# Performance work log

Hardware: AMD Instinct MI355X
Metric: run time of the kernel (lower is better)

Reference implementation:

```python
import jax, jax.numpy as jnp
import numpy as np

D = 512; H = 8; DH = D // H; DFF = 4 * D; INNER = 2 * D; K = 31
B = 8; S = 1024
EPS = 1e-5


def layer_norm(x, g, b):
    m = jnp.mean(x, axis=-1, keepdims=True)
    v = jnp.mean(jnp.square(x - m), axis=-1, keepdims=True)
    return (x - m) * jax.lax.rsqrt(v + EPS) * g + b


def setup_inputs() -> dict:
    key = jax.random.key(0)
    ks = iter(jax.random.split(key, 32))
    w = lambda *s: jax.random.normal(next(ks), s, dtype=jnp.float32) * 0.02
    d = {
        "x": jax.random.normal(next(ks), (B, S, D), dtype=jnp.float32),
        # FF module 1
        "ln1_g": jnp.ones((D,)), "ln1_b": jnp.zeros((D,)),
        "ff1_w1": w(DFF, D), "ff1_b1": jnp.zeros((DFF,)),
        "ff1_w2": w(D, DFF), "ff1_b2": jnp.zeros((D,)),
        # attention
        "lna_g": jnp.ones((D,)), "lna_b": jnp.zeros((D,)),
        "qkv_w": w(3 * D, D), "qkv_b": jnp.zeros((3 * D,)),
        "out_w": w(D, D), "out_b": jnp.zeros((D,)),
        # conv module
        "lnc_g": jnp.ones((D,)), "lnc_b": jnp.zeros((D,)),
        "pw1_w": w(INNER, D), "pw1_b": jnp.zeros((INNER,)),
        "dw_w": w(D, 1, K), "dw_b": jnp.zeros((D,)),
        "bn_g": jnp.ones((D,)), "bn_b": jnp.zeros((D,)),
        "bn_mean": jnp.zeros((D,)), "bn_var": jnp.ones((D,)),
        "pw2_w": w(D, D), "pw2_b": jnp.zeros((D,)),
        # FF module 2
        "ln2_g": jnp.ones((D,)), "ln2_b": jnp.zeros((D,)),
        "ff2_w1": w(DFF, D), "ff2_b1": jnp.zeros((DFF,)),
        "ff2_w2": w(D, DFF), "ff2_b2": jnp.zeros((D,)),
        # final layer norm
        "lnf_g": jnp.ones((D,)), "lnf_b": jnp.zeros((D,)),
    }
    return d


def _ff(x, g, b, w1, b1, w2, b2):
    h = layer_norm(x, g, b)
    h = jax.nn.silu(h @ w1.T + b1)
    h = h @ w2.T + b2
    return h + x  # FeedForwardModule adds its own residual


def _attn(x, g, b, qkv_w, qkv_b, out_w, out_b):
    h = layer_norm(x, g, b)
    qkv = (h @ qkv_w.T + qkv_b).reshape(B, S, 3, H, DH)
    q, k, v = qkv[:, :, 0], qkv[:, :, 1], qkv[:, :, 2]  # [B,S,H,DH]
    scores = jnp.einsum('bqhd,bkhd->bhqk', q, k) / np.sqrt(DH).astype(np.float32)
    probs = jax.nn.softmax(scores, axis=-1)
    ctx = jnp.einsum('bhqk,bkhd->bqhd', probs, v).reshape(B, S, D)
    return ctx @ out_w.T + out_b


def _conv(x, g, b, pw1_w, pw1_b, dw_w, dw_b, bn_g, bn_b, bn_mean, bn_var, pw2_w, pw2_b):
    h = layer_norm(x, g, b)
    y = h @ pw1_w.T + pw1_b                      # [B,S,2D] pointwise conv1
    a, gate = jnp.split(y, 2, axis=-1)           # GLU along channel dim
    y = a * jax.nn.sigmoid(gate)                 # [B,S,D]
    y = y.transpose(0, 2, 1)                     # [B,D,S]
    y = jax.lax.conv_general_dilated(
        y, dw_w, window_strides=(1,), padding=((K // 2, K // 2),),
        dimension_numbers=('NCH', 'OIH', 'NCH'), feature_group_count=D)
    y = y + dw_b[None, :, None]
    y = (y - bn_mean[None, :, None]) * jax.lax.rsqrt(bn_var + EPS)[None, :, None]
    y = y * bn_g[None, :, None] + bn_b[None, :, None]
    y = jax.nn.silu(y)
    y = y.transpose(0, 2, 1)                     # [B,S,D]
    y = y @ pw2_w.T + pw2_b
    return y + x  # ConvModule adds its own residual


def reference(x, ln1_g, ln1_b, ff1_w1, ff1_b1, ff1_w2, ff1_b2,
              lna_g, lna_b, qkv_w, qkv_b, out_w, out_b,
              lnc_g, lnc_b, pw1_w, pw1_b, dw_w, dw_b,
              bn_g, bn_b, bn_mean, bn_var, pw2_w, pw2_b,
              ln2_g, ln2_b, ff2_w1, ff2_b1, ff2_w2, ff2_b2,
              lnf_g, lnf_b):
    x = x + 0.5 * _ff(x, ln1_g, ln1_b, ff1_w1, ff1_b1, ff1_w2, ff1_b2)
    x = x + _attn(x, lna_g, lna_b, qkv_w, qkv_b, out_w, out_b)
    x = x + _conv(x, lnc_g, lnc_b, pw1_w, pw1_b, dw_w, dw_b,
                  bn_g, bn_b, bn_mean, bn_var, pw2_w, pw2_b)
    x = x + 0.5 * _ff(x, ln2_g, ln2_b, ff2_w1, ff2_b1, ff2_w2, ff2_b2)
    return layer_norm(x, lnf_g, lnf_b)
```

## Files before the change

### kernel.cpp

```cpp
#include <hip/hip_runtime.h>
#include <hip/hip_bf16.h>

typedef __attribute__((ext_vector_type(8))) short bf16x8;
typedef __attribute__((ext_vector_type(4))) float f32x4;

#define NTOK 8192
#define SEQ  1024
#define NH   8

__device__ __forceinline__ float bfs2f(short s) {
  union { unsigned u; float f; } x; x.u = ((unsigned)(unsigned short)s) << 16; return x.f;
}
__device__ __forceinline__ short f2bfs(float f) {
  __hip_bfloat16 h = __float2bfloat16(f);
  return *reinterpret_cast<short*>(&h);
}
__device__ __forceinline__ float bfp2f(const __hip_bfloat16* p) {
  return bfs2f(*reinterpret_cast<const short*>(p));
}

__device__ __forceinline__ void gld16(const void* g, void* l) {
  __builtin_amdgcn_global_load_lds(
      (__attribute__((address_space(1))) void*)const_cast<void*>(g),
      (__attribute__((address_space(3))) void*)l, 16, 0, 0);
}

__global__ __launch_bounds__(256) void cvt_x_kernel(const float* __restrict__ xin,
                                                    float* __restrict__ xs) {
  const size_t i = ((size_t)blockIdx.x * 256 + threadIdx.x) * 8;
  *reinterpret_cast<f32x4*>(xs + i)     = *reinterpret_cast<const f32x4*>(xin + i);
  *reinterpret_cast<f32x4*>(xs + i + 4) = *reinterpret_cast<const f32x4*>(xin + i + 4);
}

struct WSeg { const float* src; unsigned dst_off; unsigned nvec; };
struct WPack { WSeg s[8]; };

__global__ __launch_bounds__(256) void cast_wall_kernel(WPack p,
                                                        __hip_bfloat16* __restrict__ dst) {
  unsigned v = blockIdx.x * 256 + threadIdx.x;
#pragma unroll
  for (int t = 0; t < 8; ++t) {
    if (v < p.s[t].nvec) {
      const float* s = p.s[t].src + (size_t)v * 8;
      f32x4 a = *reinterpret_cast<const f32x4*>(s);
      f32x4 b = *reinterpret_cast<const f32x4*>(s + 4);
      bf16x8 o;
#pragma unroll
      for (int j = 0; j < 4; ++j) { o[j] = f2bfs(a[j]); o[4 + j] = f2bfs(b[j]); }
      *reinterpret_cast<bf16x8*>(reinterpret_cast<short*>(dst) +
                                 (size_t)(p.s[t].dst_off + v) * 8) = o;
      return;
    }
    v -= p.s[t].nvec;
  }
}

__global__ __launch_bounds__(256) void cast_dww_kernel(const float* __restrict__ src,
                                                       __hip_bfloat16* __restrict__ dst) {
  for (int k = 0; k < 31; ++k)
    for (int c = threadIdx.x; c < 512; c += 256)
      dst[k * 512 + c] = __float2bfloat16(src[c * 31 + k]);
}

struct PtrPack { const void* p[23]; };

__global__ __launch_bounds__(256) void cast_small_kernel(PtrPack pk,
                                                         __hip_bfloat16* __restrict__ dst) {
  constexpr int sizes[23] = {512, 512, 2048, 512, 512, 512, 1536, 512, 512, 512, 1024, 512,
                             512, 512, 512, 512, 512, 512, 512, 2048, 512, 512, 512};
  int off = 0;
  for (int t = 0; t < 23; ++t) {
    const int n = sizes[t];
    for (int i = threadIdx.x; i < n; i += 256)
      dst[off + i] = __float2bfloat16(((const float*)pk.p[t])[i]);
    off += n;
  }
}

__global__ void ws_bad_kernel(float* __restrict__ out) {
  if (threadIdx.x == 0) out[0] = 5000.f;
}

__global__ __launch_bounds__(256) void ln_kernel(const float* __restrict__ in,
                                                 const __hip_bfloat16* __restrict__ g,
                                                 const __hip_bfloat16* __restrict__ b,
                                                 __hip_bfloat16* __restrict__ out) {
  const int wv = threadIdx.x >> 6, ln = threadIdx.x & 63;
  const int row = blockIdx.x * 4 + wv;
  const float* p = in + (size_t)row * 512 + ln * 8;
  float v[8];
  {
    const f32x4* p4 = reinterpret_cast<const f32x4*>(p);
    f32x4 a = p4[0], c = p4[1];
#pragma unroll
    for (int j = 0; j < 4; ++j) { v[j] = a[j]; v[4 + j] = c[j]; }
  }
  float s = 0.f;
#pragma unroll
  for (int j = 0; j < 8; ++j) s += v[j];
  for (int m = 1; m < 64; m <<= 1) s += __shfl_xor(s, m);
  const float mean = s * (1.f / 512.f);
  float q = 0.f;
#pragma unroll
  for (int j = 0; j < 8; ++j) { float d = v[j] - mean; q += d * d; }
  for (int m = 1; m < 64; m <<= 1) q += __shfl_xor(q, m);
  const float rstd = rsqrtf(q * (1.f / 512.f) + 1e-5f);
  bf16x8 gg = *reinterpret_cast<const bf16x8*>(g + ln * 8);
  bf16x8 bb = *reinterpret_cast<const bf16x8*>(b + ln * 8);
  bf16x8 ov;
#pragma unroll
  for (int j = 0; j < 8; ++j)
    ov[j] = f2bfs((v[j] - mean) * rstd * bfs2f(gg[j]) + bfs2f(bb[j]));
  *reinterpret_cast<bf16x8*>(out + (size_t)row * 512 + ln * 8) = ov;
}

__global__ __launch_bounds__(256) void lnf_kernel(const float* __restrict__ in,
                                                  const __hip_bfloat16* __restrict__ g,
                                                  const __hip_bfloat16* __restrict__ b,
                                                  float* __restrict__ out) {
  const int wv = threadIdx.x >> 6, ln = threadIdx.x & 63;
  const int row = blockIdx.x * 4 + wv;
  const float* p = in + (size_t)row * 512 + ln * 8;
  float v[8];
  {
    const f32x4* p4 = reinterpret_cast<const f32x4*>(p);
    f32x4 a = p4[0], c = p4[1];
#pragma unroll
    for (int j = 0; j < 4; ++j) { v[j] = a[j]; v[4 + j] = c[j]; }
  }
  float s = 0.f;
#pragma unroll
  for (int j = 0; j < 8; ++j) s += v[j];
  for (int m = 1; m < 64; m <<= 1) s += __shfl_xor(s, m);
  const float mean = s * (1.f / 512.f);
  float q = 0.f;
#pragma unroll
  for (int j = 0; j < 8; ++j) { float d = v[j] - mean; q += d * d; }
  for (int m = 1; m < 64; m <<= 1) q += __shfl_xor(q, m);
  const float rstd = rsqrtf(q * (1.f / 512.f) + 1e-5f);
  bf16x8 gg = *reinterpret_cast<const bf16x8*>(g + ln * 8);
  bf16x8 bb = *reinterpret_cast<const bf16x8*>(b + ln * 8);
  f32x4 o0, o1;
#pragma unroll
  for (int j = 0; j < 4; ++j) {
    o0[j] = (v[j] - mean) * rstd * bfs2f(gg[j]) + bfs2f(bb[j]);
    o1[j] = (v[4 + j] - mean) * rstd * bfs2f(gg[4 + j]) + bfs2f(bb[4 + j]);
  }
  float* op = out + (size_t)row * 512 + ln * 8;
  *reinterpret_cast<f32x4*>(op) = o0;
  *reinterpret_cast<f32x4*>(op + 4) = o1;
}

template <int EPI>
__global__ __launch_bounds__(256, 2) void gemm_bt(const __hip_bfloat16* __restrict__ A,
                                                  const __hip_bfloat16* __restrict__ W,
                                                  const __hip_bfloat16* __restrict__ bias,
                                                  __hip_bfloat16* __restrict__ outb,
                                                  float* __restrict__ resid,
                                                  int K, int M, float alpha, float beta) {
  __shared__ __align__(16) __hip_bfloat16 As[128 * 64];
  __shared__ __align__(16) __hip_bfloat16 Bs[128 * 64];
  const int tid = threadIdx.x;
  const int wv = tid >> 6, ln = tid & 63;
  const int hi = ln >> 4, lo = ln & 15;
  const int n0 = blockIdx.x * 128;
  const int m0 = blockIdx.y * 128;
  const int wr = wv >> 1, wc = wv & 1;
  const int srow = ln >> 3;
  const int scol = (ln & 7) * 8;

  f32x4 acc[4][4] = {};

  for (int k0 = 0; k0 < K; k0 += 64) {
    __syncthreads();
#pragma unroll
    for (int i = 0; i < 4; ++i) {
      const int grp = i * 4 + wv;
      const int row = grp * 8 + srow;
      gld16(A + (size_t)(n0 + row) * K + k0 + scol, As + grp * 512);
      gld16(W + (size_t)(m0 + row) * K + k0 + scol, Bs + grp * 512);
    }
    __syncthreads();
#pragma unroll
    for (int kk = 0; kk < 64; kk += 32) {
      bf16x8 af[4], bfr[4];
#pragma unroll
      for (int r = 0; r < 4; ++r)
        af[r] = *reinterpret_cast<const bf16x8*>(As + (wr * 64 + r * 16 + lo) * 64 + kk + hi * 8);
#pragma unroll
      for (int c = 0; c < 4; ++c)
        bfr[c] = *reinterpret_cast<const bf16x8*>(Bs + (wc * 64 + c * 16 + lo) * 64 + kk + hi * 8);
#pragma unroll
      for (int r = 0; r < 4; ++r)
#pragma unroll
        for (int c = 0; c < 4; ++c)
          acc[r][c] = __builtin_amdgcn_mfma_f32_16x16x32_bf16(af[r], bfr[c], acc[r][c], 0, 0, 0);
    }
  }

#pragma unroll
  for (int r = 0; r < 4; ++r) {
#pragma unroll
    for (int c = 0; c < 4; ++c) {
      const int m = m0 + wc * 64 + c * 16 + lo;
      const float bv = bfp2f(bias + m);
#pragma unroll
      for (int j = 0; j < 4; ++j) {
        const int n = n0 + wr * 64 + r * 16 + hi * 4 + j;
        float v = acc[r][c][j] + bv;
        if constexpr (EPI == 1) v = v / (1.f + __expf(-v));
        if constexpr (EPI <= 1) {
          outb[(size_t)n * M + m] = __float2bfloat16(v);
        } else {
          const size_t idx = (size_t)n * 512 + m;
          resid[idx] = alpha * resid[idx] + beta * v;
        }
      }
    }
  }
}

__global__ __launch_bounds__(256, 4) void gemm64_resid(const __hip_bfloat16* __restrict__ A,
                                                       const __hip_bfloat16* __restrict__ W,
                                                       const __hip_bfloat16* __restrict__ bias,
                                                       float* __restrict__ resid,
                                                       int K, float alpha, float beta) {
  __shared__ __align__(16) __hip_bfloat16 As[64 * 64];
  __shared__ __align__(16) __hip_bfloat16 Bs[128 * 64];
  const int tid = threadIdx.x;
  const int wv = tid >> 6, ln = tid & 63;
  const int hi = ln >> 4, lo = ln & 15;
  const int n0 = blockIdx.x * 64;
  const int m0 = blockIdx.y * 128;
  const int wr = wv >> 1, wc = wv & 1;
  const int srow = ln >> 3;
  const int scol = (ln & 7) * 8;

  f32x4 acc[2][4] = {};

  for (int k0 = 0; k0 < K; k0 += 64) {
    __syncthreads();
#pragma unroll
    for (int i = 0; i < 2; ++i) {
      const int grp = i * 4 + wv;
      gld16(A + (size_t)(n0 + grp * 8 + srow) * K + k0 + scol, As + grp * 512);
    }
#pragma unroll
    for (int i = 0; i < 4; ++i) {
      const int grp = i * 4 + wv;
      gld16(W + (size_t)(m0 + grp * 8 + srow) * K + k0 + scol, Bs + grp * 512);
    }
    __syncthreads();
#pragma unroll
    for (int kk = 0; kk < 64; kk += 32) {
      bf16x8 af[2], bfr[4];
#pragma unroll
      for (int r = 0; r < 2; ++r)
        af[r] = *reinterpret_cast<const bf16x8*>(As + (wr * 32 + r * 16 + lo) * 64 + kk + hi * 8);
#pragma unroll
      for (int c = 0; c < 4; ++c)
        bfr[c] = *reinterpret_cast<const bf16x8*>(Bs + (wc * 64 + c * 16 + lo) * 64 + kk + hi * 8);
#pragma unroll
      for (int r = 0; r < 2; ++r)
#pragma unroll
        for (int c = 0; c < 4; ++c)
          acc[r][c] = __builtin_amdgcn_mfma_f32_16x16x32_bf16(af[r], bfr[c], acc[r][c], 0, 0, 0);
    }
  }

#pragma unroll
  for (int r = 0; r < 2; ++r) {
#pragma unroll
    for (int c = 0; c < 4; ++c) {
      const int m = m0 + wc * 64 + c * 16 + lo;
      const float bv = bfp2f(bias + m);
#pragma unroll
      for (int j = 0; j < 4; ++j) {
        const int n = n0 + wr * 32 + r * 16 + hi * 4 + j;
        const size_t idx = (size_t)n * 512 + m;
        resid[idx] = alpha * resid[idx] + beta * (acc[r][c][j] + bv);
      }
    }
  }
}

__global__ __launch_bounds__(256, 1) void naive_attn_kernel(
    const __hip_bfloat16* __restrict__ qkv, __hip_bfloat16* __restrict__ ctx) {
  const int idx = blockIdx.x * 256 + threadIdx.x;
  const int b = idx >> 13;
  const int h = (idx >> 10) & 7;
  const int q = idx & 1023;
  const __hip_bfloat16* qp = qkv + (size_t)(b * SEQ + q) * 1536 + h * 64;
  float qreg[64];
#pragma unroll
  for (int j8 = 0; j8 < 8; ++j8) {
    bf16x8 v = *reinterpret_cast<const bf16x8*>(qp + j8 * 8);
#pragma unroll
    for (int jj = 0; jj < 8; ++jj) qreg[j8 * 8 + jj] = bfs2f(v[jj]);
  }
  float m = -1e30f, l = 0.f;
  float acc[64];
#pragma unroll
  for (int d = 0; d < 64; ++d) acc[d] = 0.f;
  for (int k = 0; k < SEQ; ++k) {
    const __hip_bfloat16* kp = qkv + (size_t)(b * SEQ + k) * 1536 + 512 + h * 64;
    float dot = 0.f;
#pragma unroll
    for (int j8 = 0; j8 < 8; ++j8) {
      bf16x8 v = *reinterpret_cast<const bf16x8*>(kp + j8 * 8);
#pragma unroll
      for (int jj = 0; jj < 8; ++jj) dot += qreg[j8 * 8 + jj] * bfs2f(v[jj]);
    }
    const float s = dot * 0.125f;
    const float nm = fmaxf(m, s);
    const float resc = __expf(m - nm);
    const float p = __expf(s - nm);
    l = l * resc + p;
    const __hip_bfloat16* vp = qkv + (size_t)(b * SEQ + k) * 1536 + 1024 + h * 64;
#pragma unroll
    for (int j8 = 0; j8 < 8; ++j8) {
      bf16x8 v = *reinterpret_cast<const bf16x8*>(vp + j8 * 8);
#pragma unroll
      for (int jj = 0; jj < 8; ++jj)
        acc[j8 * 8 + jj] = acc[j8 * 8 + jj] * resc + p * bfs2f(v[jj]);
    }
    m = nm;
  }
  __hip_bfloat16* op = ctx + (size_t)(b * SEQ + q) * 512 + h * 64;
  const float rl = 1.f / l;
#pragma unroll
  for (int j8 = 0; j8 < 8; ++j8) {
    bf16x8 o;
#pragma unroll
    for (int jj = 0; jj < 8; ++jj) o[jj] = f2bfs(acc[j8 * 8 + jj] * rl);
    *reinterpret_cast<bf16x8*>(op + j8 * 8) = o;
  }
}

__global__ __launch_bounds__(256) void vtrans_kernel(const __hip_bfloat16* __restrict__ qkv,
                                                     __hip_bfloat16* __restrict__ vT) {
  __shared__ __hip_bfloat16 tile[64][65];
  const int bh = blockIdx.x;
  const int s0 = blockIdx.y * 64;
  const int b = bh >> 3, h = bh & 7;
  const int c = threadIdx.x & 63;
  const int r4 = threadIdx.x >> 6;
#pragma unroll
  for (int i = 0; i < 16; ++i) {
    const int s = r4 * 16 + i;
    tile[s][c] = qkv[(size_t)(b * 1024 + s0 + s) * 1536 + 1024 + h * 64 + c];
  }
  __syncthreads();
#pragma unroll
  for (int i = 0; i < 16; ++i) {
    const int d = r4 * 16 + i;
    vT[((size_t)bh * 64 + d) * 1024 + s0 + c] = tile[c][d];
  }
}

__global__ __launch_bounds__(256, 4) void attn_kernel(const __hip_bfloat16* __restrict__ qkv,
                                                      const __hip_bfloat16* __restrict__ vT,
                                                      __hip_bfloat16* __restrict__ ctx) {
  __shared__ __align__(16) short Ks[2][64 * 64];
  __shared__ __align__(16) short Vs[2][64 * 64];
  __shared__ __align__(16) short P[4][16][64];
  const int tid = threadIdx.x;
  const int wv = tid >> 6, ln = tid & 63;
  const int hi = ln >> 4, lo = ln & 15;
  const int lo7 = lo & 7;
  const int blk = ((blockIdx.x & 7) << 7) | (blockIdx.x >> 3);
  const int qt = blk & 15, h = (blk >> 4) & 7, b = blk >> 7;
  const int q0 = qt * 64 + wv * 16;
  const float scale = 0.125f;

  const int srow8 = ln >> 3;
  const int gsrc = (ln & 7) ^ srow8;

  const __hip_bfloat16* qp = qkv + (size_t)(b * SEQ + q0 + lo) * 1536 + h * 64 + hi * 8;
  bf16x8 aq0 = *reinterpret_cast<const bf16x8*>(qp);
  bf16x8 aq1 = *reinterpret_cast<const bf16x8*>(qp + 32);

  const __hip_bfloat16* kbase = qkv + 512 + h * 64 + (size_t)b * SEQ * 1536;
  const __hip_bfloat16* vbase = vT + (size_t)(b * NH + h) * 64 * 1024;

  f32x4 oacc[4] = {};
  float mrow[4] = {-1e30f, -1e30f, -1e30f, -1e30f};
  float lrow[4] = {0.f, 0.f, 0.f, 0.f};

#pragma unroll
  for (int c = 0; c < 2; ++c) {
    const int r = c * 32 + wv * 8 + srow8;
    gld16(kbase + (size_t)r * 1536 + gsrc * 8, &Ks[0][(c * 32 + wv * 8) * 64]);
    gld16(vbase + (size_t)r * 1024 + gsrc * 8, &Vs[0][(c * 32 + wv * 8) * 64]);
  }
  __syncthreads();

  int cb = 0;
  for (int kt = 0; kt < 16; ++kt) {
    if (kt < 15) {
      const int kb2 = (kt + 1) * 64;
#pragma unroll
      for (int c = 0; c < 2; ++c) {
        const int r = c * 32 + wv * 8 + srow8;
        gld16(kbase + (size_t)(kb2 + r) * 1536 + gsrc * 8,
              &Ks[cb ^ 1][(c * 32 + wv * 8) * 64]);
        gld16(vbase + (size_t)r * 1024 + kb2 + gsrc * 8,
              &Vs[cb ^ 1][(c * 32 + wv * 8) * 64]);
      }
    }

    f32x4 sc[4] = {};
#pragma unroll
    for (int nt = 0; nt < 4; ++nt) {
      const short* kr = &Ks[cb][(nt * 16 + lo) * 64];
      bf16x8 bk0 = *reinterpret_cast<const bf16x8*>(kr + ((hi ^ lo7) << 3));
      bf16x8 bk1 = *reinterpret_cast<const bf16x8*>(kr + (((hi + 4) ^ lo7) << 3));
      sc[nt] = __builtin_amdgcn_mfma_f32_16x16x32_bf16(aq0, bk0, sc[nt], 0, 0, 0);
      sc[nt] = __builtin_amdgcn_mfma_f32_16x16x32_bf16(aq1, bk1, sc[nt], 0, 0, 0);
    }

#pragma unroll
    for (int j = 0; j < 4; ++j) {
      float v = fmaxf(fmaxf(sc[0][j], sc[1][j]), fmaxf(sc[2][j], sc[3][j])) * scale;
      v = fmaxf(v, __shfl_xor(v, 1));
      v = fmaxf(v, __shfl_xor(v, 2));
      v = fmaxf(v, __shfl_xor(v, 4));
      v = fmaxf(v, __shfl_xor(v, 8));
      const float nm = fmaxf(mrow[j], v);
      const float resc = __expf(mrow[j] - nm);
      mrow[j] = nm;
      const int prow = hi * 4 + j;
      const int pswz = (prow & 7) << 3;
      float rs = 0.f;
#pragma unroll
      for (int nt = 0; nt < 4; ++nt) {
        const float p = __expf(sc[nt][j] * scale - nm);
        P[wv][prow][(nt * 16 + lo) ^ pswz] = f2bfs(p);
        rs += p;
      }
      rs += __shfl_xor(rs, 1);
      rs += __shfl_xor(rs, 2);
      rs += __shfl_xor(rs, 4);
      rs += __shfl_xor(rs, 8);
      lrow[j] = lrow[j] * resc + rs;
#pragma unroll
      for (int dt = 0; dt < 4; ++dt) oacc[dt][j] *= resc;
    }
    __syncthreads();

    const short* pr = &P[wv][lo][0];
    bf16x8 ap0 = *reinterpret_cast<const bf16x8*>(pr + ((hi ^ lo7) << 3));
    bf16x8 ap1 = *reinterpret_cast<const bf16x8*>(pr + (((hi + 4) ^ lo7) << 3));
#pragma unroll
    for (int dt = 0; dt < 4; ++dt) {
      const short* vr = &Vs[cb][(dt * 16 + lo) * 64];
      bf16x8 bv0 = *reinterpret_cast<const bf16x8*>(vr + ((hi ^ lo7) << 3));
      bf16x8 bv1 = *reinterpret_cast<const bf16x8*>(vr + (((hi + 4) ^ lo7) << 3));
      oacc[dt] = __builtin_amdgcn_mfma_f32_16x16x32_bf16(ap0, bv0, oacc[dt], 0, 0, 0);
      oacc[dt] = __builtin_amdgcn_mfma_f32_16x16x32_bf16(ap1, bv1, oacc[dt], 0, 0, 0);
    }
    __syncthreads();
    cb ^= 1;
  }
#pragma unroll
  for (int dt = 0; dt < 4; ++dt)
#pragma unroll
    for (int j = 0; j < 4; ++j) {
      const int n = b * SEQ + q0 + hi * 4 + j;
      const int d = h * 64 + dt * 16 + lo;
      ctx[(size_t)n * 512 + d] = __float2bfloat16(oacc[dt][j] / lrow[j]);
    }
}

__global__ __launch_bounds__(256) void glu8_kernel(const __hip_bfloat16* __restrict__ y,
                                                   __hip_bfloat16* __restrict__ o) {
  const int i = blockIdx.x * 256 + threadIdx.x;
  const int c8 = i & 63;
  const int n = i >> 6;
  const short* yp = reinterpret_cast<const short*>(y) + (size_t)n * 1024 + c8 * 8;
  bf16x8 a = *reinterpret_cast<const bf16x8*>(yp);
  bf16x8 g = *reinterpret_cast<const bf16x8*>(yp + 512);
  bf16x8 ov;
#pragma unroll
  for (int j = 0; j < 8; ++j) {
    const float av = bfs2f(a[j]);
    const float gv = bfs2f(g[j]);
    ov[j] = f2bfs(av / (1.f + __expf(-gv)));
  }
  *reinterpret_cast<bf16x8*>(reinterpret_cast<short*>(o) + (size_t)n * 512 + c8 * 8) = ov;
}

__global__ __launch_bounds__(256) void dwconv8_kernel(const __hip_bfloat16* __restrict__ cin,
                                                      const __hip_bfloat16* __restrict__ wkT,
                                                      const __hip_bfloat16* __restrict__ cb,
                                                      const __hip_bfloat16* __restrict__ bng,
                                                      const __hip_bfloat16* __restrict__ bnb,
                                                      const __hip_bfloat16* __restrict__ bnm,
                                                      const __hip_bfloat16* __restrict__ bnv,
                                                      __hip_bfloat16* __restrict__ outp) {
  const int i = blockIdx.x * 256 + threadIdx.x;
  const int c8 = i & 63;
  const int n = i >> 6;
  const int t = n & 1023;
  const int base = n - t;
  const int co = c8 * 8;

  float acc[8];
  {
    bf16x8 bv = *reinterpret_cast<const bf16x8*>(cb + co);
#pragma unroll
    for (int j = 0; j < 8; ++j) acc[j] = bfs2f(bv[j]);
  }
  const int k0 = (t >= 15) ? 0 : (15 - t);
  const int k1 = (t <= SEQ - 16) ? 31 : (SEQ - 1 - t + 16);
  const short* cin_s = reinterpret_cast<const short*>(cin);
  const short* wk_s = reinterpret_cast<const short*>(wkT);
  for (int k = k0; k < k1; ++k) {
    const int ts = t + k - 15;
    bf16x8 xv = *reinterpret_cast<const bf16x8*>(cin_s + (((size_t)(base + ts)) << 9) + co);
    bf16x8 wv = *reinterpret_cast<const bf16x8*>(wk_s + k * 512 + co);
#pragma unroll
    for (int j = 0; j < 8; ++j) acc[j] += bfs2f(xv[j]) * bfs2f(wv[j]);
  }
  bf16x8 g = *reinterpret_cast<const bf16x8*>(bng + co);
  bf16x8 bb = *reinterpret_cast<const bf16x8*>(bnb + co);
  bf16x8 bm = *reinterpret_cast<const bf16x8*>(bnm + co);
  bf16x8 bvv = *reinterpret_cast<const bf16x8*>(bnv + co);
  bf16x8 ov;
#pragma unroll
  for (int j = 0; j < 8; ++j) {
    const float scl = bfs2f(g[j]) * rsqrtf(bfs2f(bvv[j]) + 1e-5f);
    float v = (acc[j] - bfs2f(bm[j])) * scl + bfs2f(bb[j]);
    v = v / (1.f + __expf(-v));
    ov[j] = f2bfs(v);
  }
  *reinterpret_cast<bf16x8*>(reinterpret_cast<short*>(outp) + ((size_t)n << 9) + co) = ov;
}

extern "C" void kernel_launch(void* const* d_in, const int* in_sizes, int n_in,
                              void* d_out, int out_size, void* d_ws, size_t ws_size,
                              hipStream_t stream) {
  float* out = (float*)d_out;
  if (ws_size < ((size_t)80 << 20)) {
    ws_bad_kernel<<<1, 64, 0, stream>>>(out);
    return;
  }

  char* ws = (char*)d_ws;
  float*          xs = (float*)ws;
  __hip_bfloat16* t0 = (__hip_bfloat16*)(ws + ((size_t)16 << 20));
  __hip_bfloat16* t1 = (__hip_bfloat16*)(ws + ((size_t)24 << 20));
  __hip_bfloat16* t2 = (__hip_bfloat16*)(ws + ((size_t)56 << 20));
  __hip_bfloat16* wc = (__hip_bfloat16*)(ws + ((size_t)64 << 20));
  __hip_bfloat16* vT = t1 + (size_t)NTOK * 1536;

  __hip_bfloat16* wc_ff1_w1 = wc + 0;
  __hip_bfloat16* wc_ff1_w2 = wc + 1048576;
  __hip_bfloat16* wc_qkv_w  = wc + 2097152;
  __hip_bfloat16* wc_out_w  = wc + 2883584;
  __hip_bfloat16* wc_pw1_w  = wc + 3145728;
  __hip_bfloat16* wc_pw2_w  = wc + 3670016;
  __hip_bfloat16* wc_ff2_w1 = wc + 3932160;
  __hip_bfloat16* wc_ff2_w2 = wc + 4980736;
  __hip_bfloat16* wc_dwT    = wc + 6029312;
  __hip_bfloat16* sm        = wc + 6045184;
  __hip_bfloat16* c_ln1_g = sm + 0,     *c_ln1_b = sm + 512,   *c_ff1_b1 = sm + 1024;
  __hip_bfloat16* c_ff1_b2 = sm + 3072, *c_lna_g = sm + 3584,  *c_lna_b = sm + 4096;
  __hip_bfloat16* c_qkv_b = sm + 4608,  *c_out_b = sm + 6144,  *c_lnc_g = sm + 6656;
  __hip_bfloat16* c_lnc_b = sm + 7168,  *c_pw1_b = sm + 7680,  *c_dw_b = sm + 8704;
  __hip_bfloat16* c_bn_g = sm + 9216,   *c_bn_b = sm + 9728,   *c_bn_m = sm + 10240;
  __hip_bfloat16* c_bn_v = sm + 10752,  *c_pw2_b = sm + 11264, *c_ln2_g = sm + 11776;
  __hip_bfloat16* c_ln2_b = sm + 12288, *c_ff2_b1 = sm + 12800, *c_ff2_b2 = sm + 14848;
  __hip_bfloat16* c_lnf_g = sm + 15360, *c_lnf_b = sm + 15872;

  cvt_x_kernel<<<2048, 256, 0, stream>>>((const float*)d_in[0], xs);
  {
    WPack wp;
    wp.s[0] = {(const float*)d_in[3],  0,      131072};
    wp.s[1] = {(const float*)d_in[5],  131072, 131072};
    wp.s[2] = {(const float*)d_in[9],  262144, 98304};
    wp.s[3] = {(const float*)d_in[11], 360448, 32768};
    wp.s[4] = {(const float*)d_in[15], 393216, 65536};
    wp.s[5] = {(const float*)d_in[23], 458752, 32768};
    wp.s[6] = {(const float*)d_in[27], 491520, 131072};
    wp.s[7] = {(const float*)d_in[29], 622592, 131072};
    cast_wall_kernel<<<2944, 256, 0, stream>>>(wp, wc);
  }
  cast_dww_kernel<<<1, 256, 0, stream>>>((const float*)d_in[17], wc_dwT);
  PtrPack pk;
  const int small_idx[23] = {1, 2, 4, 6, 7, 8, 10, 12, 13, 14, 16, 18,
                             19, 20, 21, 22, 24, 25, 26, 28, 30, 31, 32};
  for (int t = 0; t < 23; ++t) pk.p[t] = d_in[small_idx[t]];
  cast_small_kernel<<<1, 256, 0, stream>>>(pk, sm);

  ln_kernel<<<2048, 256, 0, stream>>>(xs, c_ln1_g, c_ln1_b, t0);
  gemm_bt<1><<<dim3(64, 16), 256, 0, stream>>>(t0, wc_ff1_w1, c_ff1_b1, t1, nullptr, 512, 2048, 0.f, 0.f);
  gemm64_resid<<<dim3(128, 4), 256, 0, stream>>>(t1, wc_ff1_w2, c_ff1_b2, xs, 2048, 1.5f, 0.5f);

  ln_kernel<<<2048, 256, 0, stream>>>(xs, c_lna_g, c_lna_b, t0);
  gemm_bt<0><<<dim3(64, 12), 256, 0, stream>>>(t0, wc_qkv_w, c_qkv_b, t1, nullptr, 512, 1536, 0.f, 0.f);
  vtrans_kernel<<<dim3(64, 16), 256, 0, stream>>>(t1, vT);
  attn_kernel<<<1024, 256, 0, stream>>>(t1, vT, t2);
  gemm64_resid<<<dim3(128, 4), 256, 0, stream>>>(t2, wc_out_w, c_out_b, xs, 512, 1.0f, 1.0f);

  ln_kernel<<<2048, 256, 0, stream>>>(xs, c_lnc_g, c_lnc_b, t0);
  gemm_bt<0><<<dim3(64, 8), 256, 0, stream>>>(t0, wc_pw1_w, c_pw1_b, t1, nullptr, 512, 1024, 0.f, 0.f);
  glu8_kernel<<<2048, 256, 0, stream>>>(t1, t2);
  dwconv8_kernel<<<2048, 256, 0, stream>>>(t2, wc_dwT, c_dw_b, c_bn_g, c_bn_b, c_bn_m, c_bn_v, t0);
  gemm64_resid<<<dim3(128, 4), 256, 0, stream>>>(t0, wc_pw2_w, c_pw2_b, xs, 512, 2.0f, 1.0f);

  ln_kernel<<<2048, 256, 0, stream>>>(xs, c_ln2_g, c_ln2_b, t0);
  gemm_bt<1><<<dim3(64, 16), 256, 0, stream>>>(t0, wc_ff2_w1, c_ff2_b1, t1, nullptr, 512, 2048, 0.f, 0.f);
  gemm64_resid<<<dim3(128, 4), 256, 0, stream>>>(t1, wc_ff2_w2, c_ff2_b2, xs, 2048, 1.5f, 0.5f);

  lnf_kernel<<<2048, 256, 0, stream>>>(xs, c_lnf_g, c_lnf_b, out);
}
```

Measured before the change: 358.0 us.

## Drop input copy, remap GEMM workgroups per XCD, prescale Q, relax attention barrier

Removes the kernel that copied x into the residual workspace. The first LayerNorm and the first residual GEMM now read the input directly, using a new source pointer so the residual can be read from one buffer and written to another. Both GEMM kernels remap workgroup IDs so that consecutive tiles land on the same XCD, aiming for better L2 reuse of A and W tiles. In attention, Q is prescaled by 1/8 in bf16 at load, which drops per-score multiplies but adds a rounding step. A __syncthreads before reading P is replaced by a compiler-only barrier, relying on each wave reading only its own P slice.

```diff
diff --git a/kernel.cpp b/kernel.cpp
--- a/kernel.cpp
+++ b/kernel.cpp
@@ -23,13 +23,6 @@
   __builtin_amdgcn_global_load_lds(
       (__attribute__((address_space(1))) void*)const_cast<void*>(g),
       (__attribute__((address_space(3))) void*)l, 16, 0, 0);
-}
-
-__global__ __launch_bounds__(256) void cvt_x_kernel(const float* __restrict__ xin,
-                                                    float* __restrict__ xs) {
-  const size_t i = ((size_t)blockIdx.x * 256 + threadIdx.x) * 8;
-  *reinterpret_cast<f32x4*>(xs + i)     = *reinterpret_cast<const f32x4*>(xin + i);
-  *reinterpret_cast<f32x4*>(xs + i + 4) = *reinterpret_cast<const f32x4*>(xin + i + 4);
 }
 
 struct WSeg { const float* src; unsigned dst_off; unsigned nvec; };
@@ -163,8 +156,12 @@
   const int tid = threadIdx.x;
   const int wv = tid >> 6, ln = tid & 63;
   const int hi = ln >> 4, lo = ln & 15;
-  const int n0 = blockIdx.x * 128;
-  const int m0 = blockIdx.y * 128;
+  const int gx = gridDim.x;
+  const int nwg = gx * gridDim.y;
+  const int t = blockIdx.y * gx + blockIdx.x;
+  const int w = (t & 7) * (nwg >> 3) + (t >> 3);
+  const int n0 = (w & (gx - 1)) * 128;
+  const int m0 = (w / gx) * 128;
   const int wr = wv >> 1, wc = wv & 1;
   const int srow = ln >> 3;
   const int scol = (ln & 7) * 8;
@@ -223,6 +220,7 @@
 __global__ __launch_bounds__(256, 4) void gemm64_resid(const __hip_bfloat16* __restrict__ A,
                                                        const __hip_bfloat16* __restrict__ W,
                                                        const __hip_bfloat16* __restrict__ bias,
+                                                       const float* __restrict__ rsrc,
                                                        float* __restrict__ resid,
                                                        int K, float alpha, float beta) {
   __shared__ __align__(16) __hip_bfloat16 As[64 * 64];
@@ -230,8 +228,12 @@
   const int tid = threadIdx.x;
   const int wv = tid >> 6, ln = tid & 63;
   const int hi = ln >> 4, lo = ln & 15;
-  const int n0 = blockIdx.x * 64;
-  const int m0 = blockIdx.y * 128;
+  const int gx = gridDim.x;
+  const int nwg = gx * gridDim.y;
+  const int t = blockIdx.y * gx + blockIdx.x;
+  const int w = (t & 7) * (nwg >> 3) + (t >> 3);
+  const int n0 = (w & (gx - 1)) * 64;
+  const int m0 = (w / gx) * 128;
   const int wr = wv >> 1, wc = wv & 1;
   const int srow = ln >> 3;
   const int scol = (ln & 7) * 8;
@@ -278,7 +280,7 @@
       for (int j = 0; j < 4; ++j) {
         const int n = n0 + wr * 32 + r * 16 + hi * 4 + j;
         const size_t idx = (size_t)n * 512 + m;
-        resid[idx] = alpha * resid[idx] + beta * (acc[r][c][j] + bv);
+        resid[idx] = alpha * rsrc[idx] + beta * (acc[r][c][j] + bv);
       }
     }
   }
@@ -371,14 +373,21 @@
   const int blk = ((blockIdx.x & 7) << 7) | (blockIdx.x >> 3);
   const int qt = blk & 15, h = (blk >> 4) & 7, b = blk >> 7;
   const int q0 = qt * 64 + wv * 16;
-  const float scale = 0.125f;
 
   const int srow8 = ln >> 3;
   const int gsrc = (ln & 7) ^ srow8;
 
-  const __hip_bfloat16* qp = qkv + (size_t)(b * SEQ + q0 + lo) * 1536 + h * 64 + hi * 8;
-  bf16x8 aq0 = *reinterpret_cast<const bf16x8*>(qp);
-  bf16x8 aq1 = *reinterpret_cast<const bf16x8*>(qp + 32);
+  bf16x8 aq0, aq1;
+  {
+    const __hip_bfloat16* qp = qkv + (size_t)(b * SEQ + q0 + lo) * 1536 + h * 64 + hi * 8;
+    bf16x8 r0 = *reinterpret_cast<const bf16x8*>(qp);
+    bf16x8 r1 = *reinterpret_cast<const bf16x8*>(qp + 32);
+#pragma unroll
+    for (int j = 0; j < 8; ++j) {
+      aq0[j] = f2bfs(bfs2f(r0[j]) * 0.125f);
+      aq1[j] = f2bfs(bfs2f(r1[j]) * 0.125f);
+    }
+  }
 
   const __hip_bfloat16* kbase = qkv + 512 + h * 64 + (size_t)b * SEQ * 1536;
   const __hip_bfloat16* vbase = vT + (size_t)(b * NH + h) * 64 * 1024;
@@ -421,7 +430,7 @@
 
 #pragma unroll
     for (int j = 0; j < 4; ++j) {
-      float v = fmaxf(fmaxf(sc[0][j], sc[1][j]), fmaxf(sc[2][j], sc[3][j])) * scale;
+      float v = fmaxf(fmaxf(sc[0][j], sc[1][j]), fmaxf(sc[2][j], sc[3][j]));
       v = fmaxf(v, __shfl_xor(v, 1));
       v = fmaxf(v, __shfl_xor(v, 2));
       v = fmaxf(v, __shfl_xor(v, 4));
@@ -434,7 +443,7 @@
       float rs = 0.f;
 #pragma unroll
       for (int nt = 0; nt < 4; ++nt) {
-        const float p = __expf(sc[nt][j] * scale - nm);
+        const float p = __expf(sc[nt][j] - nm);
         P[wv][prow][(nt * 16 + lo) ^ pswz] = f2bfs(p);
         rs += p;
       }
@@ -446,7 +455,7 @@
 #pragma unroll
       for (int dt = 0; dt < 4; ++dt) oacc[dt][j] *= resc;
     }
-    __syncthreads();
+    asm volatile("" ::: "memory");
 
     const short* pr = &P[wv][lo][0];
     bf16x8 ap0 = *reinterpret_cast<const bf16x8*>(pr + ((hi ^ lo7) << 3));
@@ -545,6 +554,8 @@
     ws_bad_kernel<<<1, 64, 0, stream>>>(out);
     return;
   }
+
+  const float* x = (const float*)d_in[0];
 
   char* ws = (char*)d_ws;
   float*          xs = (float*)ws;
@@ -573,7 +584,6 @@
   __hip_bfloat16* c_ln2_b = sm + 12288, *c_ff2_b1 = sm + 12800, *c_ff2_b2 = sm + 14848;
   __hip_bfloat16* c_lnf_g = sm + 15360, *c_lnf_b = sm + 15872;
 
-  cvt_x_kernel<<<2048, 256, 0, stream>>>((const float*)d_in[0], xs);
   {
     WPack wp;
     wp.s[0] = {(const float*)d_in[3],  0,      131072};
@@ -593,25 +603,25 @@
   for (int t = 0; t < 23; ++t) pk.p[t] = d_in[small_idx[t]];
   cast_small_kernel<<<1, 256, 0, stream>>>(pk, sm);
 
-  ln_kernel<<<2048, 256, 0, stream>>>(xs, c_ln1_g, c_ln1_b, t0);
+  ln_kernel<<<2048, 256, 0, stream>>>(x, c_ln1_g, c_ln1_b, t0);
   gemm_bt<1><<<dim3(64, 16), 256, 0, stream>>>(t0, wc_ff1_w1, c_ff1_b1, t1, nullptr, 512, 2048, 0.f, 0.f);
-  gemm64_resid<<<dim3(128, 4), 256, 0, stream>>>(t1, wc_ff1_w2, c_ff1_b2, xs, 2048, 1.5f, 0.5f);
+  gemm64_resid<<<dim3(128, 4), 256, 0, stream>>>(t1, wc_ff1_w2, c_ff1_b2, x, xs, 2048, 1.5f, 0.5f);
 
   ln_kernel<<<2048, 256, 0, stream>>>(xs, c_lna_g, c_lna_b, t0);
   gemm_bt<0><<<dim3(64, 12), 256, 0, stream>>>(t0, wc_qkv_w, c_qkv_b, t1, nullptr, 512, 1536, 0.f, 0.f);
   vtrans_kernel<<<dim3(64, 16), 256, 0, stream>>>(t1, vT);
   attn_kernel<<<1024, 256, 0, stream>>>(t1, vT, t2);
-  gemm64_resid<<<dim3(128, 4), 256, 0, stream>>>(t2, wc_out_w, c_out_b, xs, 512, 1.0f, 1.0f);
+  gemm64_resid<<<dim3(128, 4), 256, 0, stream>>>(t2, wc_out_w, c_out_b, xs, xs, 512, 1.0f, 1.0f);
 
   ln_kernel<<<2048, 256, 0, stream>>>(xs, c_lnc_g, c_lnc_b, t0);
   gemm_bt<0><<<dim3(64, 8), 256, 0, stream>>>(t0, wc_pw1_w, c_pw1_b, t1, nullptr, 512, 1024, 0.f, 0.f);
   glu8_kernel<<<2048, 256, 0, stream>>>(t1, t2);
   dwconv8_kernel<<<2048, 256, 0, stream>>>(t2, wc_dwT, c_dw_b, c_bn_g, c_bn_b, c_bn_m, c_bn_v, t0);
-  gemm64_resid<<<dim3(128, 4), 256, 0, stream>>>(t0, wc_pw2_w, c_pw2_b, xs, 512, 2.0f, 1.0f);
+  gemm64_resid<<<dim3(128, 4), 256, 0, stream>>>(t0, wc_pw2_w, c_pw2_b, xs, xs, 512, 2.0f, 1.0f);
 
   ln_kernel<<<2048, 256, 0, stream>>>(xs, c_ln2_g, c_ln2_b, t0);
   gemm_bt<1><<<dim3(64, 16), 256, 0, stream>>>(t0, wc_ff2_w1, c_ff2_b1, t1, nullptr, 512, 2048, 0.f, 0.f);
-  gemm64_resid<<<dim3(128, 4), 256, 0, stream>>>(t1, wc_ff2_w2, c_ff2_b2, xs, 2048, 1.5f, 0.5f);
+  gemm64_resid<<<dim3(128, 4), 256, 0, stream>>>(t1, wc_ff2_w2, c_ff2_b2, xs, xs, 2048, 1.5f, 0.5f);
 
   lnf_kernel<<<2048, 256, 0, stream>>>(xs, c_lnf_g, c_lnf_b, out);
 }
```

Result: no change. 359.0 us (+0.3%).
